# Kernel optimization log

Hardware: AMD Instinct MI355X
Metric: run time of the kernel (lower is better)

Reference implementation:

```python
import jax, jax.numpy as jnp
import numpy as np

N_HEAD = 16


def setup_inputs() -> dict:
    key = jax.random.key(0)
    k0, k1, k2, k3 = jax.random.split(key, 4)
    B, T, C = 2, 2048, 1024
    scale = 0.02
    x = jax.random.normal(k0, (B, T, C), dtype=jnp.float32)
    W_attn = jax.random.normal(k1, (C, 3 * C), dtype=jnp.float32) * scale
    b_attn = jnp.zeros((3 * C,), dtype=jnp.float32)
    W_proj = jax.random.normal(k2, (C, C), dtype=jnp.float32) * scale
    b_proj = jnp.zeros((C,), dtype=jnp.float32)
    return {"x": x, "W_attn": W_attn, "b_attn": b_attn, "W_proj": W_proj, "b_proj": b_proj}


def reference(x, W_attn, b_attn, W_proj, b_proj):
    B, T, C = x.shape
    H = N_HEAD
    hd = C // H
    # fused qkv projection
    qkv = x @ W_attn + b_attn                      # [B, T, 3C]
    q, k, v = jnp.split(qkv, 3, axis=-1)
    q = q.reshape(B, T, H, hd).transpose(0, 2, 1, 3)  # [B, H, T, hd]
    k = k.reshape(B, T, H, hd).transpose(0, 2, 1, 3)
    v = v.reshape(B, T, H, hd).transpose(0, 2, 1, 3)
    # scaled dot-product attention with causal mask (past_kv=None -> seq_len == T)
    att = jnp.einsum('bhqd,bhkd->bhqk', q, k) / jnp.sqrt(jnp.float32(hd))
    causal = jnp.tril(jnp.ones((T, T), dtype=bool))  # [T, T]
    att = jnp.where(causal[None, None, :, :], att, jnp.float32(-jnp.inf))
    att = jax.nn.softmax(att, axis=-1)
    y = jnp.einsum('bhqk,bhkd->bhqd', att, v)        # [B, H, T, hd]
    y = y.transpose(0, 2, 1, 3).reshape(B, T, C)
    y = y @ W_proj + b_proj
    return (y, k, v)  # (output, present_k, present_v)
```

## Files before the change

### kernel.cpp

```cpp
#include <hip/hip_runtime.h>
#include <hip/hip_bf16.h>

typedef __bf16 bf16;
typedef __bf16 bf16x8 __attribute__((ext_vector_type(8)));
typedef float f32x4 __attribute__((ext_vector_type(4)));
typedef unsigned int u32;

#define MFMA_BF16(a, b, c) __builtin_amdgcn_mfma_f32_16x16x32_bf16((a), (b), (c), 0, 0, 0)

#define SEQ_T 2048
#define DIM_C 1024

__device__ inline void gload16(const void* g, void* l) {
  __builtin_amdgcn_global_load_lds((const __attribute__((address_space(1))) u32*)g,
                                   (__attribute__((address_space(3))) u32*)l, 16, 0, 0);
}

__global__ __launch_bounds__(256) void prep_kernel(
    const float* __restrict__ x, const float* __restrict__ Wa,
    const float* __restrict__ Wp, bf16* __restrict__ xbf,
    bf16* __restrict__ wat, bf16* __restrict__ wpt) {
  const int tid = threadIdx.x;
  const int bid = blockIdx.x;
  if (bid < 2048) {
    const size_t i = ((size_t)bid * 256 + tid) * 8;
    const f32x4 a = *(const f32x4*)(x + i);
    const f32x4 b = *(const f32x4*)(x + i + 4);
    bf16x8 r;
    r[0] = (bf16)a[0]; r[1] = (bf16)a[1]; r[2] = (bf16)a[2]; r[3] = (bf16)a[3];
    r[4] = (bf16)b[0]; r[5] = (bf16)b[1]; r[6] = (bf16)b[2]; r[7] = (bf16)b[3];
    *(bf16x8*)(xbf + i) = r;
  } else if (bid < 3584) {
    const int cid = (bid - 2048) * 256 + tid;
    const int kg = cid / 3072, n = cid - kg * 3072;
    bf16x8 r;
#pragma unroll
    for (int j = 0; j < 8; j++) r[j] = (bf16)Wa[(size_t)(kg * 8 + j) * 3072 + n];
    *(bf16x8*)(wat + (size_t)cid * 8) = r;
  } else {
    const int cid = (bid - 3584) * 256 + tid;
    const int kg = cid >> 10, n = cid & 1023;
    bf16x8 r;
#pragma unroll
    for (int j = 0; j < 8; j++) r[j] = (bf16)Wp[(size_t)(kg * 8 + j) * 1024 + n];
    *(bf16x8*)(wpt + (size_t)cid * 8) = r;
  }
}

template <int MODE, int BM>
__global__ __launch_bounds__(256) void gemm_kernel(
    const bf16* __restrict__ A, const bf16* __restrict__ Wt,
    const float* __restrict__ bias, float* __restrict__ out0,
    float* __restrict__ out1, bf16* __restrict__ bq, bf16* __restrict__ bk2,
    bf16* __restrict__ bv2, int M, int N, int K) {
  constexpr int MI = BM / 32;
  constexpr int CA = BM / 64;
  __shared__ bf16 As[BM][32];
  __shared__ bf16 Bt[128][32];

  const int tid = threadIdx.x;
  const int wid = tid >> 6, lane = tid & 63;
  const int quad = lane >> 4, l16 = lane & 15;
  const int wm = (wid >> 1) * (BM / 2), wn = (wid & 1) * 64;
  const int m0 = blockIdx.y * BM, n0 = blockIdx.x * 128;
  const int lr = lane >> 2, lks = lane & 3;

  const f32x4 zero = {0.f, 0.f, 0.f, 0.f};
  f32x4 acc[MI][4];
#pragma unroll
  for (int i = 0; i < MI; i++)
#pragma unroll
    for (int j = 0; j < 4; j++) acc[i][j] = zero;

  for (int kk = 0; kk < K; kk += 32) {
    __syncthreads();
#pragma unroll
    for (int p = 0; p < CA; p++) {
      const int c = wid * CA + p;
      gload16(A + (size_t)(m0 + c * 16 + lr) * K + kk + lks * 8,
              (bf16*)As + c * 512);
    }
#pragma unroll
    for (int p = 0; p < 2; p++) {
      const int c = wid * 2 + p;
      gload16(Wt + ((size_t)((kk >> 3) + lks) * N + n0 + c * 16 + lr) * 8,
              (bf16*)Bt + c * 512);
    }
    __syncthreads();
    bf16x8 af[MI], bfr[4];
#pragma unroll
    for (int i = 0; i < MI; i++)
      af[i] = *(const bf16x8*)&As[wm + i * 16 + l16][quad * 8];
#pragma unroll
    for (int j = 0; j < 4; j++)
      bfr[j] = *(const bf16x8*)&Bt[wn + j * 16 + l16][quad * 8];
#pragma unroll
    for (int i = 0; i < MI; i++)
#pragma unroll
      for (int j = 0; j < 4; j++)
        acc[i][j] = MFMA_BF16(af[i], bfr[j], acc[i][j]);
  }

#pragma unroll
  for (int i = 0; i < MI; i++) {
#pragma unroll
    for (int j = 0; j < 4; j++) {
      const int col = n0 + wn + j * 16 + l16;
      const float bv = bias[col];
#pragma unroll
      for (int r = 0; r < 4; r++) {
        const int gm = m0 + wm + i * 16 + quad * 4 + r;
        const float v = acc[i][j][r] + bv;
        if (MODE == 0) {
          out0[(size_t)gm * N + col] = v;
        } else {
          const int which = col >> 10, c = col & 1023;
          const int h = c >> 6, d = c & 63;
          const int b = gm >> 11, t = gm & (SEQ_T - 1);
          const size_t idx = ((size_t)(b * 16 + h) * SEQ_T + t) * 64 + d;
          if (which == 0) {
            bq[idx] = (bf16)(v * 0.18033688f);
          } else if (which == 1) {
            out0[idx] = v;
            bk2[idx] = (bf16)v;
          } else {
            out1[idx] = v;
            bv2[idx] = (bf16)v;
          }
        }
      }
    }
  }
}

__global__ __launch_bounds__(512) void attn_kernel(
    const bf16* __restrict__ Qbf, const bf16* __restrict__ Kbf,
    const bf16* __restrict__ V, bf16* __restrict__ Y) {
  __shared__ bf16 Ks[2][64 * 72];
  __shared__ bf16 Vt[2][64 * 72];
  __shared__ bf16 Ps[8 * 16 * 72];

  const int tid = threadIdx.x;
  const int wid = tid >> 6, lane = tid & 63;
  const int quad = lane >> 4, l16 = lane & 15;

  const int qt = (blockIdx.y < 16) ? ((int)gridDim.x - 1 - (int)blockIdx.x)
                                   : (int)blockIdx.x;
  const int bh = blockIdx.y;
  const int q0 = qt * 128;
  const int b = bh >> 4, h = bh & 15;

  const bf16* qp = Qbf + (size_t)bh * SEQ_T * 64;
  const bf16* kp = Kbf + (size_t)bh * SEQ_T * 64;
  const bf16* vp = V + (size_t)bh * SEQ_T * 64;

  bf16x8 aq[2];
#pragma unroll
  for (int ks = 0; ks < 2; ks++)
    aq[ks] = *(const bf16x8*)(qp + (size_t)(q0 + wid * 16 + l16) * 64 + ks * 32 + quad * 8);

  bf16x8 bones;
#pragma unroll
  for (int j = 0; j < 8; j++) bones[j] = (bf16)1.0f;

  const f32x4 zero = {0.f, 0.f, 0.f, 0.f};
  f32x4 oacc[4], lacc;
  lacc = zero;
#pragma unroll
  for (int t = 0; t < 4; t++) oacc[t] = zero;

  const int last = 2 * qt + 1;
  bf16x8 kreg, vreg;

  auto load_tile = [&](int t) {
    const size_t base = (size_t)t * 64 * 64;
    kreg = *(const bf16x8*)(kp + base + (size_t)tid * 8);
    vreg = *(const bf16x8*)(vp + base + (size_t)tid * 8);
  };
  auto stage_tile = [&](int buf) {
    const int key = tid >> 3, hs = tid & 7;
    *(bf16x8*)&Ks[buf][key * 72 + hs * 8] = kreg;
#pragma unroll
    for (int e = 0; e < 8; e++) {
      const int hr = hs * 8 + e;
      Vt[buf][hr * 72 + (((key >> 3) ^ hs) * 8) + (key & 7)] = vreg[e];
    }
  };

  load_tile(0);
  stage_tile(0);
  load_tile(1);

  for (int it = 0; it <= last; ++it) {
    const int cur = it & 1;
    __syncthreads();
    if (it < last) stage_tile(cur ^ 1);
    if (it + 1 < last) load_tile(it + 2);

    const bool skip = (it == last) && (wid < 4);
    const bool dm = (it == 2 * qt && wid < 4) || (it == last && wid >= 4);

    f32x4 sa[4];
    if (!skip) {
#pragma unroll
      for (int nt = 0; nt < 4; nt++) {
        const bf16x8 bk0 = *(const bf16x8*)&Ks[cur][(nt * 16 + l16) * 72 + quad * 8];
        const bf16x8 bk1 = *(const bf16x8*)&Ks[cur][(nt * 16 + l16) * 72 + 32 + quad * 8];
        f32x4 s = MFMA_BF16(aq[0], bk0, zero);
        sa[nt] = MFMA_BF16(aq[1], bk1, s);
      }
      if (dm) {
#pragma unroll
        for (int nt = 0; nt < 4; nt++) {
          const int col = it * 64 + nt * 16 + l16;
#pragma unroll
          for (int r = 0; r < 4; r++) {
            const int row = q0 + wid * 16 + quad * 4 + r;
            if (col > row) sa[nt][r] = -1e30f;
          }
        }
      }
      bf16* pwb = &Ps[wid * 16 * 72];
#pragma unroll
      for (int nt = 0; nt < 4; nt++) {
        const int cb = nt * 16 + l16;
#pragma unroll
        for (int r = 0; r < 4; r++) {
          const int pr = quad * 4 + r;
          pwb[pr * 72 + (((cb >> 3) ^ (pr & 7)) * 8) + (cb & 7)] = (bf16)exp2f(sa[nt][r]);
        }
      }
      bf16x8 ap[2];
#pragma unroll
      for (int ks = 0; ks < 2; ks++)
        ap[ks] = *(const bf16x8*)&pwb[l16 * 72 + (((ks * 4 + quad) ^ (l16 & 7)) * 8)];
      lacc = MFMA_BF16(ap[0], bones, lacc);
      lacc = MFMA_BF16(ap[1], bones, lacc);
#pragma unroll
      for (int nt = 0; nt < 4; nt++) {
        const int n = nt * 16 + l16;
#pragma unroll
        for (int ks = 0; ks < 2; ks++) {
          const bf16x8 bv = *(const bf16x8*)&Vt[cur][n * 72 + (((ks * 4 + quad) ^ (n >> 3)) * 8)];
          oacc[nt] = MFMA_BF16(ap[ks], bv, oacc[nt]);
        }
      }
    }
  }

  float inv[4];
#pragma unroll
  for (int r = 0; r < 4; r++) inv[r] = 1.f / lacc[r];
#pragma unroll
  for (int nt = 0; nt < 4; nt++) {
#pragma unroll
    for (int r = 0; r < 4; r++) {
      const int row = q0 + wid * 16 + quad * 4 + r;
      const int col = h * 64 + nt * 16 + l16;
      Y[((size_t)(b * SEQ_T + row)) * DIM_C + col] = (bf16)(oacc[nt][r] * inv[r]);
    }
  }
}

extern "C" void kernel_launch(void* const* d_in, const int* in_sizes, int n_in,
                              void* d_out, int out_size, void* d_ws, size_t ws_size,
                              hipStream_t stream) {
  (void)in_sizes; (void)n_in; (void)out_size; (void)ws_size;
  const float* x = (const float*)d_in[0];
  const float* W_attn = (const float*)d_in[1];
  const float* b_attn = (const float*)d_in[2];
  const float* W_proj = (const float*)d_in[3];
  const float* b_proj = (const float*)d_in[4];

  float* out = (float*)d_out;
  float* y_out = out;
  float* k_out = out + (size_t)4194304;
  float* v_out = out + (size_t)8388608;
  bf16* qbf = (bf16*)d_out;
  bf16* kbf = (bf16*)d_out + 4194304;
  bf16* y_att = (bf16*)d_in[0];
  bf16* vbf = (bf16*)d_in[0] + 4194304;
  bf16* xbf = (bf16*)d_ws;
  bf16* wat = xbf + 4194304;
  bf16* wpt = wat + 3145728;

  prep_kernel<<<4096, 256, 0, stream>>>(x, W_attn, W_proj, xbf, wat, wpt);
  gemm_kernel<1, 128><<<dim3(3072 / 128, 4096 / 128), 256, 0, stream>>>(
      xbf, wat, b_attn, k_out, v_out, qbf, kbf, vbf, 4096, 3072, 1024);
  attn_kernel<<<dim3(SEQ_T / 128, 32), 512, 0, stream>>>(qbf, kbf, vbf, y_att);
  gemm_kernel<0, 64><<<dim3(1024 / 128, 4096 / 64), 256, 0, stream>>>(
      y_att, wpt, b_proj, y_out, nullptr, nullptr, nullptr, nullptr,
      4096, 1024, 1024);
}
```

Measured before the change: 208.4 us.

## Double-buffer GEMM LDS tiles, read fp32 V directly in attention, add setprio

The GEMM k-loop now uses two LDS buffers so the next tile's async global-to-LDS load overlaps the MFMAs on the current tile, with one barrier per iteration instead of two. The QKV GEMM no longer writes a separate bf16 copy of V; attention loads the fp32 V output and converts it while staging into LDS. s_setprio is raised around MFMA blocks in attention to favour math waves. The trade-offs are more LDS use in the GEMM and doubled V read bytes in attention, against fewer stores in the GEMM.

```diff
diff --git a/kernel.cpp b/kernel.cpp
--- a/kernel.cpp
+++ b/kernel.cpp
@@ -52,11 +52,11 @@
     const bf16* __restrict__ A, const bf16* __restrict__ Wt,
     const float* __restrict__ bias, float* __restrict__ out0,
     float* __restrict__ out1, bf16* __restrict__ bq, bf16* __restrict__ bk2,
-    bf16* __restrict__ bv2, int M, int N, int K) {
+    int M, int N, int K) {
   constexpr int MI = BM / 32;
   constexpr int CA = BM / 64;
-  __shared__ bf16 As[BM][32];
-  __shared__ bf16 Bt[128][32];
+  __shared__ bf16 As[2][BM * 32];
+  __shared__ bf16 Bt[2][128 * 32];
 
   const int tid = threadIdx.x;
   const int wid = tid >> 6, lane = tid & 63;
@@ -72,33 +72,41 @@
 #pragma unroll
     for (int j = 0; j < 4; j++) acc[i][j] = zero;
 
-  for (int kk = 0; kk < K; kk += 32) {
-    __syncthreads();
+  auto stage = [&](int buf, int kk) {
 #pragma unroll
     for (int p = 0; p < CA; p++) {
       const int c = wid * CA + p;
       gload16(A + (size_t)(m0 + c * 16 + lr) * K + kk + lks * 8,
-              (bf16*)As + c * 512);
+              (bf16*)As[buf] + c * 512);
     }
 #pragma unroll
     for (int p = 0; p < 2; p++) {
       const int c = wid * 2 + p;
       gload16(Wt + ((size_t)((kk >> 3) + lks) * N + n0 + c * 16 + lr) * 8,
-              (bf16*)Bt + c * 512);
-    }
-    __syncthreads();
+              (bf16*)Bt[buf] + c * 512);
+    }
+  };
+
+  const int nt = K >> 5;
+  stage(0, 0);
+  __syncthreads();
+  int cur = 0;
+  for (int t = 0; t < nt; t++) {
+    if (t + 1 < nt) stage(cur ^ 1, (t + 1) << 5);
     bf16x8 af[MI], bfr[4];
 #pragma unroll
     for (int i = 0; i < MI; i++)
-      af[i] = *(const bf16x8*)&As[wm + i * 16 + l16][quad * 8];
+      af[i] = *(const bf16x8*)&As[cur][(wm + i * 16 + l16) * 32 + quad * 8];
 #pragma unroll
     for (int j = 0; j < 4; j++)
-      bfr[j] = *(const bf16x8*)&Bt[wn + j * 16 + l16][quad * 8];
+      bfr[j] = *(const bf16x8*)&Bt[cur][(wn + j * 16 + l16) * 32 + quad * 8];
 #pragma unroll
     for (int i = 0; i < MI; i++)
 #pragma unroll
       for (int j = 0; j < 4; j++)
         acc[i][j] = MFMA_BF16(af[i], bfr[j], acc[i][j]);
+    __syncthreads();
+    cur ^= 1;
   }
 
 #pragma unroll
@@ -125,7 +133,6 @@
             bk2[idx] = (bf16)v;
           } else {
             out1[idx] = v;
-            bv2[idx] = (bf16)v;
           }
         }
       }
@@ -135,7 +142,7 @@
 
 __global__ __launch_bounds__(512) void attn_kernel(
     const bf16* __restrict__ Qbf, const bf16* __restrict__ Kbf,
-    const bf16* __restrict__ V, bf16* __restrict__ Y) {
+    const float* __restrict__ V, bf16* __restrict__ Y) {
   __shared__ bf16 Ks[2][64 * 72];
   __shared__ bf16 Vt[2][64 * 72];
   __shared__ bf16 Ps[8 * 16 * 72];
@@ -152,7 +159,7 @@
 
   const bf16* qp = Qbf + (size_t)bh * SEQ_T * 64;
   const bf16* kp = Kbf + (size_t)bh * SEQ_T * 64;
-  const bf16* vp = V + (size_t)bh * SEQ_T * 64;
+  const float* vp = V + (size_t)bh * SEQ_T * 64;
 
   bf16x8 aq[2];
 #pragma unroll
@@ -170,20 +177,23 @@
   for (int t = 0; t < 4; t++) oacc[t] = zero;
 
   const int last = 2 * qt + 1;
-  bf16x8 kreg, vreg;
+  bf16x8 kreg;
+  f32x4 vf[2];
 
   auto load_tile = [&](int t) {
     const size_t base = (size_t)t * 64 * 64;
     kreg = *(const bf16x8*)(kp + base + (size_t)tid * 8);
-    vreg = *(const bf16x8*)(vp + base + (size_t)tid * 8);
+    vf[0] = *(const f32x4*)(vp + base + (size_t)tid * 8);
+    vf[1] = *(const f32x4*)(vp + base + (size_t)tid * 8 + 4);
   };
   auto stage_tile = [&](int buf) {
     const int key = tid >> 3, hs = tid & 7;
     *(bf16x8*)&Ks[buf][key * 72 + hs * 8] = kreg;
 #pragma unroll
     for (int e = 0; e < 8; e++) {
+      const float v = (e < 4) ? vf[0][e] : vf[1][e - 4];
       const int hr = hs * 8 + e;
-      Vt[buf][hr * 72 + (((key >> 3) ^ hs) * 8) + (key & 7)] = vreg[e];
+      Vt[buf][hr * 72 + (((key >> 3) ^ hs) * 8) + (key & 7)] = (bf16)v;
     }
   };
 
@@ -202,6 +212,7 @@
 
     f32x4 sa[4];
     if (!skip) {
+      __builtin_amdgcn_s_setprio(1);
 #pragma unroll
       for (int nt = 0; nt < 4; nt++) {
         const bf16x8 bk0 = *(const bf16x8*)&Ks[cur][(nt * 16 + l16) * 72 + quad * 8];
@@ -209,6 +220,7 @@
         f32x4 s = MFMA_BF16(aq[0], bk0, zero);
         sa[nt] = MFMA_BF16(aq[1], bk1, s);
       }
+      __builtin_amdgcn_s_setprio(0);
       if (dm) {
 #pragma unroll
         for (int nt = 0; nt < 4; nt++) {
@@ -234,6 +246,7 @@
 #pragma unroll
       for (int ks = 0; ks < 2; ks++)
         ap[ks] = *(const bf16x8*)&pwb[l16 * 72 + (((ks * 4 + quad) ^ (l16 & 7)) * 8)];
+      __builtin_amdgcn_s_setprio(1);
       lacc = MFMA_BF16(ap[0], bones, lacc);
       lacc = MFMA_BF16(ap[1], bones, lacc);
 #pragma unroll
@@ -245,6 +258,7 @@
           oacc[nt] = MFMA_BF16(ap[ks], bv, oacc[nt]);
         }
       }
+      __builtin_amdgcn_s_setprio(0);
     }
   }
 
@@ -279,16 +293,14 @@
   bf16* qbf = (bf16*)d_out;
   bf16* kbf = (bf16*)d_out + 4194304;
   bf16* y_att = (bf16*)d_in[0];
-  bf16* vbf = (bf16*)d_in[0] + 4194304;
   bf16* xbf = (bf16*)d_ws;
   bf16* wat = xbf + 4194304;
   bf16* wpt = wat + 3145728;
 
   prep_kernel<<<4096, 256, 0, stream>>>(x, W_attn, W_proj, xbf, wat, wpt);
   gemm_kernel<1, 128><<<dim3(3072 / 128, 4096 / 128), 256, 0, stream>>>(
-      xbf, wat, b_attn, k_out, v_out, qbf, kbf, vbf, 4096, 3072, 1024);
-  attn_kernel<<<dim3(SEQ_T / 128, 32), 512, 0, stream>>>(qbf, kbf, vbf, y_att);
+      xbf, wat, b_attn, k_out, v_out, qbf, kbf, 4096, 3072, 1024);
+  attn_kernel<<<dim3(SEQ_T / 128, 32), 512, 0, stream>>>(qbf, kbf, v_out, y_att);
   gemm_kernel<0, 64><<<dim3(1024 / 128, 4096 / 64), 256, 0, stream>>>(
-      y_att, wpt, b_proj, y_out, nullptr, nullptr, nullptr, nullptr,
-      4096, 1024, 1024);
-}
+      y_att, wpt, b_proj, y_out, nullptr, nullptr, nullptr, 4096, 1024, 1024);
+}
```

Measured after the change: 200.9 us. -3.6%, faster.
